# Kernel tuning notes

Hardware: AMD Instinct MI355X
Metric: run time of the kernel (lower is better)

## Reference

```python
import jax, jax.numpy as jnp
import numpy as np

B, N, D, H = 8, 1024, 512, 8
HD = D // H
SCALE = 1.0 / np.sqrt(HD).astype(np.float32)


def setup_inputs() -> dict:
    key = jax.random.key(0)
    ks = jax.random.split(key, 7)
    x = jax.random.normal(ks[0], (B, N, D), dtype=jnp.float32)
    U = jax.random.normal(ks[1], (N, N), dtype=jnp.float32)
    attn_mask = jax.random.uniform(ks[2], (B, 1, 1, N), dtype=jnp.float32)
    # learned params: qkv projection D->3D and output projection D->D (with bias)
    w_qkv = jax.random.normal(ks[3], (D, 3 * D), dtype=jnp.float32) / np.sqrt(D).astype(np.float32)
    b_qkv = jnp.zeros((3 * D,), dtype=jnp.float32)
    w_out = jax.random.normal(ks[4], (D, D), dtype=jnp.float32) / np.sqrt(D).astype(np.float32)
    b_out = jnp.zeros((D,), dtype=jnp.float32)
    return {"x": x, "U": U, "attn_mask": attn_mask,
            "w_qkv": w_qkv, "b_qkv": b_qkv, "w_out": w_out, "b_out": b_out}


def reference(x, U, attn_mask, w_qkv, b_qkv, w_out, b_out):
    # QKV projection (QuantIdentity layers are identity in math; key_value = x)
    qkv = x @ w_qkv + b_qkv                       # [B, N, 3D]
    q, k, v = jnp.split(qkv, 3, axis=-1)          # each [B, N, D]

    def split_heads(t):
        return t.reshape(B, N, H, HD).transpose(0, 2, 1, 3)  # [B, H, N, HD]

    qh, kh, vh = split_heads(q), split_heads(k), split_heads(v)
    scores = jnp.einsum('bhqd,bhkd->bhqk', qh, kh) * SCALE   # [B, H, N, N]
    scores = scores + U[None, None, :, :]                    # additive interaction bias
    scores = scores + attn_mask                              # [B,1,1,N] broadcast add
    attn = jax.nn.softmax(scores, axis=-1)
    ctx = jnp.einsum('bhqk,bhkd->bhqd', attn, vh)            # [B, H, N, HD]
    ctx = ctx.transpose(0, 2, 1, 3).reshape(B, N, D)         # merge heads
    out = ctx @ w_out + b_out                                # [B, N, D]
    return out
```

## Files before the change

### kernel.cpp

```cpp
#include <hip/hip_runtime.h>

#define DEV __device__ __forceinline__

typedef __attribute__((ext_vector_type(8))) __bf16 bf16x8;
typedef __attribute__((ext_vector_type(4))) __bf16 bf16x4;
typedef __attribute__((ext_vector_type(4))) float f32x4;
typedef __attribute__((ext_vector_type(4))) float float4v;

typedef __attribute__((address_space(1))) const void ga_void;
typedef __attribute__((address_space(3))) void la_void;

constexpr float LOG2E = 1.44269504089f;
constexpr float ATT_SCALE2 = 0.125f * 1.44269504089f;

#if __has_builtin(__builtin_amdgcn_exp2f)
#define EXP2(x) __builtin_amdgcn_exp2f(x)
#else
#define EXP2(x) exp2f(x)
#endif

DEV void gload16(const void* g, void* l) {
  __builtin_amdgcn_global_load_lds((ga_void*)g, (la_void*)l, 16, 0, 0);
}

DEV f32x4 mfma_bf16(bf16x8 a, bf16x8 b, f32x4 c) {
  return __builtin_amdgcn_mfma_f32_16x16x32_bf16(a, b, c, 0, 0, 0);
}

__global__ __launch_bounds__(256) void cast_x_kernel(
    const float* __restrict__ in, __bf16* __restrict__ out, int n4) {
  int i = blockIdx.x * blockDim.x + threadIdx.x;
  int stride = gridDim.x * blockDim.x;
  for (; i < n4; i += stride) {
    float4v v = ((const float4v*)in)[i];
    bf16x4 o;
    o[0] = (__bf16)v[0]; o[1] = (__bf16)v[1];
    o[2] = (__bf16)v[2]; o[3] = (__bf16)v[3];
    ((bf16x4*)out)[i] = o;
  }
}

__global__ __launch_bounds__(256) void transpose_cast_kernel(
    const float* __restrict__ in, __bf16* __restrict__ out, int K, int Nc) {
  __shared__ float tile[32][33];
  int bx = blockIdx.x * 32;
  int by = blockIdx.y * 32;
  int tx = threadIdx.x, ty = threadIdx.y;
#pragma unroll
  for (int i = ty; i < 32; i += 8)
    tile[i][tx] = in[(size_t)(by + i) * Nc + bx + tx];
  __syncthreads();
#pragma unroll
  for (int i = ty; i < 32; i += 8)
    out[(size_t)(bx + i) * K + by + tx] = (__bf16)tile[tx][i];
}

__global__ __launch_bounds__(256) void gemm_qkv_kernel(
    const __bf16* __restrict__ A, const __bf16* __restrict__ Bt,
    const float* __restrict__ bias,
    __bf16* __restrict__ Qo, __bf16* __restrict__ Ko, __bf16* __restrict__ Vto) {
  __shared__ __align__(16) __bf16 As[2][128 * 32];
  __shared__ __align__(16) __bf16 Bs[2][128 * 32];
  const int tid = threadIdx.x;
  const int lane = tid & 63;
  const int w = tid >> 6;
  const int lr = lane & 15, lg = lane >> 4;
  const int m0 = blockIdx.x * 128, n0 = blockIdx.y * 128;
  const int wr = w >> 1, wc = w & 1;

  f32x4 acc[4][4] = {};

  auto stage = [&](int buf, int kt) {
#pragma unroll
    for (int cc = 0; cc < 2; ++cc) {
      int c = w * 2 + cc;
      int row = c * 16 + (lane >> 2);
      int slot = (lane & 3) ^ ((row >> 1) & 3);
      gload16(A + (size_t)(m0 + row) * 512 + kt * 32 + slot * 8, &As[buf][c * 512]);
      gload16(Bt + (size_t)(n0 + row) * 512 + kt * 32 + slot * 8, &Bs[buf][c * 512]);
    }
  };

  stage(0, 0);
  __syncthreads();
  for (int kt = 0; kt < 16; ++kt) {
    int cur = kt & 1;
    if (kt < 15) stage(cur ^ 1, kt + 1);
    bf16x8 av[4], bv[4];
#pragma unroll
    for (int i = 0; i < 4; ++i) {
      int row = wr * 64 + i * 16 + lr;
      av[i] = *(const bf16x8*)&As[cur][row * 32 + ((lg ^ ((row >> 1) & 3)) * 8)];
    }
#pragma unroll
    for (int j = 0; j < 4; ++j) {
      int row = wc * 64 + j * 16 + lr;
      bv[j] = *(const bf16x8*)&Bs[cur][row * 32 + ((lg ^ ((row >> 1) & 3)) * 8)];
    }
#pragma unroll
    for (int i = 0; i < 4; ++i)
#pragma unroll
      for (int j = 0; j < 4; ++j)
        acc[i][j] = mfma_bf16(av[i], bv[j], acc[i][j]);
    __syncthreads();
  }

  const int sec = n0 >> 9;
#pragma unroll
  for (int j = 0; j < 4; ++j) {
    int n = n0 + wc * 64 + j * 16 + lr;
    float bsv = bias[n];
    int nn = n & 511;
    int h = nn >> 6, d = nn & 63;
#pragma unroll
    for (int i = 0; i < 4; ++i) {
#pragma unroll
      for (int r = 0; r < 4; ++r) {
        int m = m0 + wr * 64 + i * 16 + lg * 4 + r;
        int b = m >> 10, nr = m & 1023;
        float v = acc[i][j][r] + bsv;
        if (sec == 0)
          Qo[(((size_t)(b * 8 + h)) * 1024 + nr) * 64 + d] = (__bf16)v;
        else if (sec == 1)
          Ko[(((size_t)(b * 8 + h)) * 1024 + nr) * 64 + d] = (__bf16)v;
        else
          Vto[(((size_t)(b * 8 + h)) * 64 + d) * 1024 + nr] = (__bf16)v;
      }
    }
  }
}

__global__ __launch_bounds__(256) void gemm_out_kernel(
    const __bf16* __restrict__ A, const __bf16* __restrict__ Bt,
    const float* __restrict__ bias, float* __restrict__ out) {
  __shared__ __align__(16) __bf16 As[2][64 * 32];
  __shared__ __align__(16) __bf16 Bs[2][64 * 32];
  const int tid = threadIdx.x;
  const int lane = tid & 63;
  const int w = tid >> 6;
  const int lr = lane & 15, lg = lane >> 4;
  const int m0 = blockIdx.x * 64, n0 = blockIdx.y * 64;

  f32x4 acc[4] = {};

  auto stage = [&](int buf, int kt) {
    int row = tid >> 2;
    int sg = (tid & 3) ^ ((row >> 1) & 3);
    gload16(A + (size_t)(m0 + row) * 512 + kt * 32 + sg * 8, &As[buf][tid * 8]);
    gload16(Bt + (size_t)(n0 + row) * 512 + kt * 32 + sg * 8, &Bs[buf][tid * 8]);
  };

  stage(0, 0);
  __syncthreads();
  for (int kt = 0; kt < 16; ++kt) {
    int cur = kt & 1;
    if (kt < 15) stage(cur ^ 1, kt + 1);
    int arow = w * 16 + lr;
    bf16x8 av = *(const bf16x8*)&As[cur][arow * 32 + ((lg ^ ((arow >> 1) & 3)) * 8)];
#pragma unroll
    for (int j = 0; j < 4; ++j) {
      int brow = j * 16 + lr;
      bf16x8 bv = *(const bf16x8*)&Bs[cur][brow * 32 + ((lg ^ ((brow >> 1) & 3)) * 8)];
      acc[j] = mfma_bf16(av, bv, acc[j]);
    }
    __syncthreads();
  }

#pragma unroll
  for (int j = 0; j < 4; ++j) {
    int n = n0 + j * 16 + lr;
    float bsv = bias[n];
#pragma unroll
    for (int r = 0; r < 4; ++r) {
      int m = m0 + w * 16 + lg * 4 + r;
      out[(size_t)m * 512 + n] = acc[j][r] + bsv;
    }
  }
}

__global__ __launch_bounds__(256, 2) void attn_kernel(
    const __bf16* __restrict__ Qh, const __bf16* __restrict__ Kh,
    const __bf16* __restrict__ Vth, const float* __restrict__ U,
    const float* __restrict__ mask, __bf16* __restrict__ ctx) {
  __shared__ __align__(16) __bf16 Ks[2][64 * 64];
  __shared__ __align__(16) __bf16 Vs[2][64 * 64];
  __shared__ __align__(16) __bf16 Ps[4][2][16 * 64];
  const int tid = threadIdx.x;
  const int lane = tid & 63;
  const int w = tid >> 6;
  const int lr = lane & 15, lg = lane >> 4;
  const int bh = blockIdx.x, qp = blockIdx.y;
  const int b = bh >> 3, h = bh & 7;

  int qrow[2];
  qrow[0] = qp * 64 + w * 16 + lr;
  qrow[1] = (qp + 8) * 64 + w * 16 + lr;

  bf16x8 qf[2][2];
#pragma unroll
  for (int it = 0; it < 2; ++it) {
    const __bf16* qpt = Qh + ((size_t)bh * 1024 + qrow[it]) * 64;
    qf[it][0] = *(const bf16x8*)(qpt + lg * 8);
    qf[it][1] = *(const bf16x8*)(qpt + 32 + lg * 8);
  }

  f32x4 acc_o[2][4] = {};
  float m_run[2] = {-3e38f, -3e38f}, l_run[2] = {0.f, 0.f};

  auto stageKV = [&](int buf, int kb) {
#pragma unroll
    for (int i = 0; i < 2; ++i) {
      int gid = i * 256 + tid;
      int row = gid >> 3, slot = gid & 7;
      int sg = slot ^ (row & 7);
      gload16(Kh + ((size_t)bh * 1024 + kb * 64 + row) * 64 + sg * 8,
              &Ks[buf][(i * 256 + w * 64) * 8]);
      gload16(Vth + ((size_t)bh * 64 + row) * 1024 + kb * 64 + sg * 8,
              &Vs[buf][(i * 256 + w * 64) * 8]);
    }
  };

  const float* Uq0 = U + (size_t)qrow[0] * 1024 + lg * 4;
  const float* Uq1 = U + (size_t)qrow[1] * 1024 + lg * 4;
  const float* mq = mask + b * 1024 + lg * 4;

  stageKV(0, 0);
  __builtin_amdgcn_sched_barrier(0);
  asm volatile("s_waitcnt vmcnt(0)" ::: "memory");
  __builtin_amdgcn_s_barrier();
  asm volatile("" ::: "memory");
  __builtin_amdgcn_sched_barrier(0);

  for (int kb = 0; kb < 16; ++kb) {
    const int cur = kb & 1;
    if (kb < 15) stageKV(cur ^ 1, kb + 1);

    float4v uc[2][4], mc[4];
#pragma unroll
    for (int t = 0; t < 4; ++t) {
      mc[t] = *(const float4v*)(mq + kb * 64 + t * 16);
      uc[0][t] = *(const float4v*)(Uq0 + kb * 64 + t * 16);
      uc[1][t] = *(const float4v*)(Uq1 + kb * 64 + t * 16);
    }

    f32x4 sv[2][4];
    __builtin_amdgcn_s_setprio(1);
#pragma unroll
    for (int t = 0; t < 4; ++t) {
      int krow = t * 16 + lr;
      const __bf16* kp = &Ks[cur][krow * 64];
      int sw = krow & 7;
      bf16x8 k0 = *(const bf16x8*)(kp + ((lg ^ sw) * 8));
      bf16x8 k1 = *(const bf16x8*)(kp + (((4 + lg) ^ sw) * 8));
#pragma unroll
      for (int it = 0; it < 2; ++it) {
        f32x4 z = {0.f, 0.f, 0.f, 0.f};
        z = mfma_bf16(k0, qf[it][0], z);
        z = mfma_bf16(k1, qf[it][1], z);
        sv[it][t] = z;
      }
    }
    __builtin_amdgcn_s_setprio(0);

#pragma unroll
    for (int it = 0; it < 2; ++it) {
#pragma unroll
      for (int t = 0; t < 4; ++t)
#pragma unroll
        for (int r = 0; r < 4; ++r)
          sv[it][t][r] =
              fmaf(uc[it][t][r], LOG2E, fmaf(sv[it][t][r], ATT_SCALE2, mc[t][r] * LOG2E));

      float mt[4];
#pragma unroll
      for (int t = 0; t < 4; ++t)
        mt[t] = fmaxf(fmaxf(sv[it][t][0], sv[it][t][1]), fmaxf(sv[it][t][2], sv[it][t][3]));
      float mx = fmaxf(fmaxf(mt[0], mt[1]), fmaxf(mt[2], mt[3]));
      mx = fmaxf(mx, __shfl_xor(mx, 16));
      mx = fmaxf(mx, __shfl_xor(mx, 32));

      if (__any(mx > m_run[it] + 8.f)) {
        float mnew = fmaxf(m_run[it], mx);
        float f = EXP2(m_run[it] - mnew);
        m_run[it] = mnew;
        l_run[it] *= f;
#pragma unroll
        for (int t = 0; t < 4; ++t) acc_o[it][t] *= f;
      }

      float pt[4];
#pragma unroll
      for (int t = 0; t < 4; ++t) {
#pragma unroll
        for (int r = 0; r < 4; ++r) sv[it][t][r] = EXP2(sv[it][t][r] - m_run[it]);
        pt[t] = (sv[it][t][0] + sv[it][t][1]) + (sv[it][t][2] + sv[it][t][3]);
      }
      float ps = (pt[0] + pt[1]) + (pt[2] + pt[3]);
      ps += __shfl_xor(ps, 16);
      ps += __shfl_xor(ps, 32);
      l_run[it] += ps;

      __bf16* pw = &Ps[w][it][0];
#pragma unroll
      for (int t = 0; t < 4; ++t) {
        bf16x4 pk;
        pk[0] = (__bf16)sv[it][t][0]; pk[1] = (__bf16)sv[it][t][1];
        pk[2] = (__bf16)sv[it][t][2]; pk[3] = (__bf16)sv[it][t][3];
        int k0 = t * 16 + lg * 4;
        *(bf16x4*)&pw[lr * 64 + (k0 ^ ((lr & 7) << 3))] = pk;
      }
    }

    bf16x8 pa[2][2];
#pragma unroll
    for (int it = 0; it < 2; ++it) {
      const __bf16* pp = &Ps[w][it][lr * 64];
      int sw = lr & 7;
      pa[it][0] = *(const bf16x8*)(pp + ((lg ^ sw) * 8));
      pa[it][1] = *(const bf16x8*)(pp + (((4 + lg) ^ sw) * 8));
    }
    __builtin_amdgcn_s_setprio(1);
#pragma unroll
    for (int t = 0; t < 4; ++t) {
      int vrow = t * 16 + lr;
      const __bf16* vp = &Vs[cur][vrow * 64];
      int sw = vrow & 7;
      bf16x8 v0 = *(const bf16x8*)(vp + ((lg ^ sw) * 8));
      bf16x8 v1 = *(const bf16x8*)(vp + (((4 + lg) ^ sw) * 8));
#pragma unroll
      for (int it = 0; it < 2; ++it) {
        acc_o[it][t] = mfma_bf16(v0, pa[it][0], acc_o[it][t]);
        acc_o[it][t] = mfma_bf16(v1, pa[it][1], acc_o[it][t]);
      }
    }
    __builtin_amdgcn_s_setprio(0);

    __builtin_amdgcn_sched_barrier(0);
    asm volatile("s_waitcnt vmcnt(0)" ::: "memory");
    __builtin_amdgcn_s_barrier();
    asm volatile("" ::: "memory");
    __builtin_amdgcn_sched_barrier(0);
  }

#pragma unroll
  for (int it = 0; it < 2; ++it) {
    float inv = 1.0f / l_run[it];
    __bf16* cp = ctx + ((size_t)(b * 1024 + qrow[it])) * 512 + h * 64 + lg * 4;
#pragma unroll
    for (int t = 0; t < 4; ++t) {
      bf16x4 ov;
      ov[0] = (__bf16)(acc_o[it][t][0] * inv); ov[1] = (__bf16)(acc_o[it][t][1] * inv);
      ov[2] = (__bf16)(acc_o[it][t][2] * inv); ov[3] = (__bf16)(acc_o[it][t][3] * inv);
      *(bf16x4*)(cp + t * 16) = ov;
    }
  }
}

extern "C" void kernel_launch(void* const* d_in, const int* in_sizes, int n_in,
                              void* d_out, int out_size, void* d_ws, size_t ws_size,
                              hipStream_t stream) {
  (void)in_sizes; (void)n_in; (void)out_size; (void)ws_size;
  const float* x     = (const float*)d_in[0];
  const float* U     = (const float*)d_in[1];
  const float* mask  = (const float*)d_in[2];
  const float* w_qkv = (const float*)d_in[3];
  const float* b_qkv = (const float*)d_in[4];
  const float* w_out = (const float*)d_in[5];
  const float* b_out = (const float*)d_in[6];
  float* out = (float*)d_out;

  char* p = (char*)d_ws;
  __bf16* xb    = (__bf16*)p; p += (size_t)8192 * 512 * 2;
  __bf16* wqkvT = (__bf16*)p; p += (size_t)1536 * 512 * 2;
  __bf16* woutT = (__bf16*)p; p += (size_t)512 * 512 * 2;
  __bf16* Qh    = (__bf16*)p; p += (size_t)64 * 1024 * 64 * 2;
  __bf16* Kh    = (__bf16*)p; p += (size_t)64 * 1024 * 64 * 2;
  __bf16* Vth   = (__bf16*)p; p += (size_t)64 * 64 * 1024 * 2;
  __bf16* ctx   = (__bf16*)p; p += (size_t)8192 * 512 * 2;

  hipLaunchKernelGGL(cast_x_kernel, dim3(2048), dim3(256), 0, stream,
                     x, xb, 8192 * 512 / 4);
  hipLaunchKernelGGL(transpose_cast_kernel, dim3(48, 16), dim3(32, 8), 0, stream,
                     w_qkv, wqkvT, 512, 1536);
  hipLaunchKernelGGL(transpose_cast_kernel, dim3(16, 16), dim3(32, 8), 0, stream,
                     w_out, woutT, 512, 512);
  hipLaunchKernelGGL(gemm_qkv_kernel, dim3(64, 12), dim3(256), 0, stream,
                     xb, wqkvT, b_qkv, Qh, Kh, Vth);
  hipLaunchKernelGGL(attn_kernel, dim3(64, 8), dim3(256), 0, stream,
                     Qh, Kh, Vth, U, mask, ctx);
  hipLaunchKernelGGL(gemm_out_kernel, dim3(128, 8), dim3(256), 0, stream,
                     ctx, woutT, b_out, out);
}
```

Before: 99.01 us.

## Give each attention wave private K/V buffers and drop block barriers; merge transposes

The attention kernel now stages K and V tiles per wave into private LDS buffers using 32-key blocks. Because no wave reads another wave's data, the per-iteration block-wide s_barrier and full vmcnt(0) wait are replaced by a partial vmcnt wait, so prefetch can overlap compute. Each wave now redundantly loads the full K/V tile itself, which raises global/L2 traffic fourfold, and the loop has twice as many iterations. The two weight transpose launches are also merged into one kernel to save a launch.

Measured after the change: 113.4 us. +14.5%, slower.

```diff
diff --git a/kernel.cpp b/kernel.cpp
--- a/kernel.cpp
+++ b/kernel.cpp
@@ -40,10 +40,15 @@
   }
 }
 
-__global__ __launch_bounds__(256) void transpose_cast_kernel(
-    const float* __restrict__ in, __bf16* __restrict__ out, int K, int Nc) {
+__global__ __launch_bounds__(256) void transpose_both_kernel(
+    const float* __restrict__ wqkv, const float* __restrict__ wout,
+    __bf16* __restrict__ wqkvT, __bf16* __restrict__ woutT) {
   __shared__ float tile[32][33];
-  int bx = blockIdx.x * 32;
+  const float* in;
+  __bf16* out;
+  int Nc, bx;
+  if (blockIdx.x < 48) { in = wqkv; out = wqkvT; Nc = 1536; bx = blockIdx.x * 32; }
+  else                 { in = wout; out = woutT; Nc = 512;  bx = (blockIdx.x - 48) * 32; }
   int by = blockIdx.y * 32;
   int tx = threadIdx.x, ty = threadIdx.y;
 #pragma unroll
@@ -52,7 +57,7 @@
   __syncthreads();
 #pragma unroll
   for (int i = ty; i < 32; i += 8)
-    out[(size_t)(bx + i) * K + by + tx] = (__bf16)tile[tx][i];
+    out[(size_t)(bx + i) * 512 + by + tx] = (__bf16)tile[tx][i];
 }
 
 __global__ __launch_bounds__(256) void gemm_qkv_kernel(
@@ -182,8 +187,8 @@
     const __bf16* __restrict__ Qh, const __bf16* __restrict__ Kh,
     const __bf16* __restrict__ Vth, const float* __restrict__ U,
     const float* __restrict__ mask, __bf16* __restrict__ ctx) {
-  __shared__ __align__(16) __bf16 Ks[2][64 * 64];
-  __shared__ __align__(16) __bf16 Vs[2][64 * 64];
+  __shared__ __align__(16) __bf16 Ks[4][2][32 * 64];
+  __shared__ __align__(16) __bf16 Vs[4][2][64 * 32];
   __shared__ __align__(16) __bf16 Ps[4][2][16 * 64];
   const int tid = threadIdx.x;
   const int lane = tid & 63;
@@ -209,14 +214,20 @@
 
   auto stageKV = [&](int buf, int kb) {
 #pragma unroll
-    for (int i = 0; i < 2; ++i) {
-      int gid = i * 256 + tid;
-      int row = gid >> 3, slot = gid & 7;
+    for (int i = 0; i < 4; ++i) {
+      int g = i * 64 + lane;
+      int row = g >> 3, slot = g & 7;
       int sg = slot ^ (row & 7);
-      gload16(Kh + ((size_t)bh * 1024 + kb * 64 + row) * 64 + sg * 8,
-              &Ks[buf][(i * 256 + w * 64) * 8]);
-      gload16(Vth + ((size_t)bh * 64 + row) * 1024 + kb * 64 + sg * 8,
-              &Vs[buf][(i * 256 + w * 64) * 8]);
+      gload16(Kh + ((size_t)bh * 1024 + kb * 32 + row) * 64 + sg * 8,
+              &Ks[w][buf][i * 512]);
+    }
+#pragma unroll
+    for (int i = 0; i < 4; ++i) {
+      int g = i * 64 + lane;
+      int row = g >> 2, slot = g & 3;
+      int c = (slot - ((row >> 1) & 3)) & 3;
+      gload16(Vth + ((size_t)bh * 64 + row) * 1024 + kb * 32 + c * 8,
+              &Vs[w][buf][i * 512]);
     }
   };
 
@@ -225,30 +236,35 @@
   const float* mq = mask + b * 1024 + lg * 4;
 
   stageKV(0, 0);
-  __builtin_amdgcn_sched_barrier(0);
-  asm volatile("s_waitcnt vmcnt(0)" ::: "memory");
-  __builtin_amdgcn_s_barrier();
-  asm volatile("" ::: "memory");
-  __builtin_amdgcn_sched_barrier(0);
-
-  for (int kb = 0; kb < 16; ++kb) {
+
+  for (int kb = 0; kb < 32; ++kb) {
     const int cur = kb & 1;
-    if (kb < 15) stageKV(cur ^ 1, kb + 1);
-
-    float4v uc[2][4], mc[4];
-#pragma unroll
-    for (int t = 0; t < 4; ++t) {
-      mc[t] = *(const float4v*)(mq + kb * 64 + t * 16);
-      uc[0][t] = *(const float4v*)(Uq0 + kb * 64 + t * 16);
-      uc[1][t] = *(const float4v*)(Uq1 + kb * 64 + t * 16);
-    }
-
-    f32x4 sv[2][4];
+
+    float4v uc[2][2], mc[2];
+#pragma unroll
+    for (int t = 0; t < 2; ++t) {
+      mc[t] = *(const float4v*)(mq + kb * 32 + t * 16);
+      uc[0][t] = *(const float4v*)(Uq0 + kb * 32 + t * 16);
+      uc[1][t] = *(const float4v*)(Uq1 + kb * 32 + t * 16);
+    }
+    __builtin_amdgcn_sched_barrier(0);
+
+    if (kb < 31) {
+      stageKV(cur ^ 1, kb + 1);
+      __builtin_amdgcn_sched_barrier(0);
+      asm volatile("s_waitcnt vmcnt(14)" ::: "memory");
+    } else {
+      __builtin_amdgcn_sched_barrier(0);
+      asm volatile("s_waitcnt vmcnt(6)" ::: "memory");
+    }
+    __builtin_amdgcn_sched_barrier(0);
+
+    f32x4 sv[2][2];
     __builtin_amdgcn_s_setprio(1);
 #pragma unroll
-    for (int t = 0; t < 4; ++t) {
+    for (int t = 0; t < 2; ++t) {
       int krow = t * 16 + lr;
-      const __bf16* kp = &Ks[cur][krow * 64];
+      const __bf16* kp = &Ks[w][cur][krow * 64];
       int sw = krow & 7;
       bf16x8 k0 = *(const bf16x8*)(kp + ((lg ^ sw) * 8));
       bf16x8 k1 = *(const bf16x8*)(kp + (((4 + lg) ^ sw) * 8));
@@ -265,17 +281,15 @@
 #pragma unroll
     for (int it = 0; it < 2; ++it) {
 #pragma unroll
-      for (int t = 0; t < 4; ++t)
+      for (int t = 0; t < 2; ++t)
 #pragma unroll
         for (int r = 0; r < 4; ++r)
           sv[it][t][r] =
               fmaf(uc[it][t][r], LOG2E, fmaf(sv[it][t][r], ATT_SCALE2, mc[t][r] * LOG2E));
 
-      float mt[4];
-#pragma unroll
-      for (int t = 0; t < 4; ++t)
-        mt[t] = fmaxf(fmaxf(sv[it][t][0], sv[it][t][1]), fmaxf(sv[it][t][2], sv[it][t][3]));
-      float mx = fmaxf(fmaxf(mt[0], mt[1]), fmaxf(mt[2], mt[3]));
+      float m01 = fmaxf(fmaxf(sv[it][0][0], sv[it][0][1]), fmaxf(sv[it][0][2], sv[it][0][3]));
+      float m23 = fmaxf(fmaxf(sv[it][1][0], sv[it][1][1]), fmaxf(sv[it][1][2], sv[it][1][3]));
+      float mx = fmaxf(m01, m23);
       mx = fmaxf(mx, __shfl_xor(mx, 16));
       mx = fmaxf(mx, __shfl_xor(mx, 32));
 
@@ -288,58 +302,46 @@
         for (int t = 0; t < 4; ++t) acc_o[it][t] *= f;
       }
 
-      float pt[4];
-#pragma unroll
-      for (int t = 0; t < 4; ++t) {
+      float pt[2];
+#pragma unroll
+      for (int t = 0; t < 2; ++t) {
 #pragma unroll
         for (int r = 0; r < 4; ++r) sv[it][t][r] = EXP2(sv[it][t][r] - m_run[it]);
         pt[t] = (sv[it][t][0] + sv[it][t][1]) + (sv[it][t][2] + sv[it][t][3]);
       }
-      float ps = (pt[0] + pt[1]) + (pt[2] + pt[3]);
+      float ps = pt[0] + pt[1];
       ps += __shfl_xor(ps, 16);
       ps += __shfl_xor(ps, 32);
       l_run[it] += ps;
 
       __bf16* pw = &Ps[w][it][0];
 #pragma unroll
-      for (int t = 0; t < 4; ++t) {
+      for (int t = 0; t < 2; ++t) {
         bf16x4 pk;
         pk[0] = (__bf16)sv[it][t][0]; pk[1] = (__bf16)sv[it][t][1];
         pk[2] = (__bf16)sv[it][t][2]; pk[3] = (__bf16)sv[it][t][3];
-        int k0 = t * 16 + lg * 4;
-        *(bf16x4*)&pw[lr * 64 + (k0 ^ ((lr & 7) << 3))] = pk;
-      }
-    }
-
-    bf16x8 pa[2][2];
+        int k0i = t * 16 + lg * 4;
+        *(bf16x4*)&pw[lr * 64 + (k0i ^ ((lr & 7) << 3))] = pk;
+      }
+    }
+
+    bf16x8 pa[2];
 #pragma unroll
     for (int it = 0; it < 2; ++it) {
       const __bf16* pp = &Ps[w][it][lr * 64];
-      int sw = lr & 7;
-      pa[it][0] = *(const bf16x8*)(pp + ((lg ^ sw) * 8));
-      pa[it][1] = *(const bf16x8*)(pp + (((4 + lg) ^ sw) * 8));
+      pa[it] = *(const bf16x8*)(pp + ((lg ^ (lr & 7)) * 8));
     }
     __builtin_amdgcn_s_setprio(1);
 #pragma unroll
     for (int t = 0; t < 4; ++t) {
       int vrow = t * 16 + lr;
-      const __bf16* vp = &Vs[cur][vrow * 64];
-      int sw = vrow & 7;
-      bf16x8 v0 = *(const bf16x8*)(vp + ((lg ^ sw) * 8));
-      bf16x8 v1 = *(const bf16x8*)(vp + (((4 + lg) ^ sw) * 8));
-#pragma unroll
-      for (int it = 0; it < 2; ++it) {
-        acc_o[it][t] = mfma_bf16(v0, pa[it][0], acc_o[it][t]);
-        acc_o[it][t] = mfma_bf16(v1, pa[it][1], acc_o[it][t]);
-      }
+      int vs = (lg + ((vrow >> 1) & 3)) & 3;
+      bf16x8 vf = *(const bf16x8*)(&Vs[w][cur][vrow * 32 + vs * 8]);
+#pragma unroll
+      for (int it = 0; it < 2; ++it)
+        acc_o[it][t] = mfma_bf16(vf, pa[it], acc_o[it][t]);
     }
     __builtin_amdgcn_s_setprio(0);
-
-    __builtin_amdgcn_sched_barrier(0);
-    asm volatile("s_waitcnt vmcnt(0)" ::: "memory");
-    __builtin_amdgcn_s_barrier();
-    asm volatile("" ::: "memory");
-    __builtin_amdgcn_sched_barrier(0);
   }
 
 #pragma unroll
@@ -380,10 +382,8 @@
 
   hipLaunchKernelGGL(cast_x_kernel, dim3(2048), dim3(256), 0, stream,
                      x, xb, 8192 * 512 / 4);
-  hipLaunchKernelGGL(transpose_cast_kernel, dim3(48, 16), dim3(32, 8), 0, stream,
-                     w_qkv, wqkvT, 512, 1536);
-  hipLaunchKernelGGL(transpose_cast_kernel, dim3(16, 16), dim3(32, 8), 0, stream,
-                     w_out, woutT, 512, 512);
+  hipLaunchKernelGGL(transpose_both_kernel, dim3(64, 16), dim3(32, 8), 0, stream,
+                     w_qkv, w_out, wqkvT, woutT);
   hipLaunchKernelGGL(gemm_qkv_kernel, dim3(64, 12), dim3(256), 0, stream,
                      xb, wqkvT, b_qkv, Qh, Kh, Vth);
   hipLaunchKernelGGL(attn_kernel, dim3(64, 8), dim3(256), 0, stream,
```
